# Kernel tuning notes

Measured on AMD Instinct MI355X. Metric: run time of the kernel, lower is better.

## Reference

```python
import jax, jax.numpy as jnp
import numpy as np

N = 100000   # nodes
E = 800000   # edges
D = 64       # feature dim (input=hidden=output)
EPS = 1e-5   # BatchNorm eps


def setup_inputs() -> dict:
    key = jax.random.key(0)
    ks = jax.random.split(key, 24)
    s = 1.0 / np.sqrt(D)
    inp = {
        "x": jax.random.normal(ks[0], (N, D), jnp.float32),
        "edge_index": jax.random.randint(ks[1], (2, E), 0, N, jnp.int64),
        # GCNConv weights (x @ W + b after normalized aggregation)
        "W1": jax.random.normal(ks[2], (D, D), jnp.float32) * s,
        "b1": jax.random.normal(ks[3], (D,), jnp.float32) * 0.01,
        "W2": jax.random.normal(ks[4], (D, D), jnp.float32) * s,
        "b2": jax.random.normal(ks[5], (D,), jnp.float32) * 0.01,
        "W3": jax.random.normal(ks[6], (D, D), jnp.float32) * s,
        "b3": jax.random.normal(ks[7], (D,), jnp.float32) * 0.01,
        # BatchNorm1d (inference: running stats)
        "bn1_g": jax.random.uniform(ks[8], (D,), jnp.float32, 0.5, 1.5),
        "bn1_b": jax.random.normal(ks[9], (D,), jnp.float32) * 0.1,
        "bn1_m": jax.random.normal(ks[10], (D,), jnp.float32) * 0.1,
        "bn1_v": jax.random.uniform(ks[11], (D,), jnp.float32, 0.5, 1.5),
        "bn2_g": jax.random.uniform(ks[12], (D,), jnp.float32, 0.5, 1.5),
        "bn2_b": jax.random.normal(ks[13], (D,), jnp.float32) * 0.1,
        "bn2_m": jax.random.normal(ks[14], (D,), jnp.float32) * 0.1,
        "bn2_v": jax.random.uniform(ks[15], (D,), jnp.float32, 0.5, 1.5),
        # predictor MLP: Linear -> tanh -> (dropout=id) -> Linear
        "pW1": jax.random.normal(ks[16], (D, D), jnp.float32) * s,
        "pb1": jax.random.normal(ks[17], (D,), jnp.float32) * 0.01,
        "pW2": jax.random.normal(ks[18], (D, D), jnp.float32) * s,
        "pb2": jax.random.normal(ks[19], (D,), jnp.float32) * 0.01,
    }
    return inp


def _gcn_norm(edge_index):
    # add self loops, compute sym-normalized edge coefficients (PyG GCNConv)
    loop = jnp.arange(N, dtype=edge_index.dtype)
    src = jnp.concatenate([edge_index[0], loop])
    dst = jnp.concatenate([edge_index[1], loop])
    deg = jax.ops.segment_sum(jnp.ones(src.shape[0], jnp.float32), dst, num_segments=N)
    dis = jax.lax.rsqrt(deg)  # deg >= 1 due to self loops
    norm = dis[src] * dis[dst]
    return src, dst, norm


def _gcn_layer(x, src, dst, norm, W, b):
    h = x @ W                              # [N, D] small GEMM
    msg = h[src] * norm[:, None]           # [E+N, D] gather (memory bound)
    return jax.ops.segment_sum(msg, dst, num_segments=N) + b  # scatter-add


def _bn(x, g, b, m, v):
    return (x - m) * (g * jax.lax.rsqrt(v + EPS)) + b


def reference(x, edge_index, W1, b1, W2, b2, W3, b3,
              bn1_g, bn1_b, bn1_m, bn1_v, bn2_g, bn2_b, bn2_m, bn2_v,
              pW1, pb1, pW2, pb2):
    src, dst, norm = _gcn_norm(edge_index)
    h = _gcn_layer(x, src, dst, norm, W1, b1)
    h = jax.nn.relu(_bn(h, bn1_g, bn1_b, bn1_m, bn1_v))   # dropout = id (eval)
    h = _gcn_layer(h, src, dst, norm, W2, b2)
    h = jax.nn.relu(_bn(h, bn2_g, bn2_b, bn2_m, bn2_v))
    h = _gcn_layer(h, src, dst, norm, W3, b3)
    out = jnp.tanh(h @ pW1 + pb1) @ pW2 + pb2              # predictor MLP
    return out
```

## Files before the change

kernel.cpp:

```cpp
#include <hip/hip_runtime.h>
#include <hip/hip_fp16.h>

#define N_NODES 100000
#define N_EDGES 800000
#define DIM 64
#define BN_EPS 1e-5f
#define LDX 68
#define EDGE_CAP 1600000

__global__ __launch_bounds__(256) void k_cvt_count(const float* __restrict__ x,
                                                   __half* __restrict__ xh,
                                                   const int* __restrict__ dst,
                                                   int* __restrict__ deg,
                                                   int* __restrict__ rank) {
    int idx = blockIdx.x * blockDim.x + threadIdx.x;
    if (idx < 1600000) {
        float4 v = ((const float4*)x)[idx];
        unsigned int u0 = __half_as_ushort(__float2half(v.x));
        unsigned int u1 = __half_as_ushort(__float2half(v.y));
        unsigned int u2 = __half_as_ushort(__float2half(v.z));
        unsigned int u3 = __half_as_ushort(__float2half(v.w));
        ((uint2*)xh)[idx] = make_uint2(u0 | (u1 << 16), u2 | (u3 << 16));
    }
    if (idx < N_EDGES) rank[idx] = atomicAdd(&deg[dst[idx]], 1);
}

__global__ __launch_bounds__(256) void k_scan_fuse(const int* __restrict__ deg,
                                                   int* __restrict__ row_off,
                                                   float* __restrict__ dinv,
                                                   int* __restrict__ gcount,
                                                   const float* __restrict__ W3,
                                                   const float* __restrict__ b3,
                                                   const float* __restrict__ pW1,
                                                   const float* __restrict__ pb1,
                                                   float* __restrict__ W3p,
                                                   float* __restrict__ b3p) {
    int tid = threadIdx.x;
    if (blockIdx.x == 98) {
        int c = tid & 63;
        int kbase = (tid >> 6) * 16;
        for (int k = kbase; k < kbase + 16; ++k) {
            float acc = 0.f;
#pragma unroll 8
            for (int j = 0; j < 64; ++j)
                acc = fmaf(W3[k * 64 + j], pW1[j * 64 + c], acc);
            W3p[k * 64 + c] = acc;
        }
        if (tid < 64) {
            float acc = pb1[c];
#pragma unroll 8
            for (int j = 0; j < 64; ++j)
                acc = fmaf(b3[j], pW1[j * 64 + c], acc);
            b3p[c] = acc;
        }
        return;
    }
    __shared__ int sdata[256];
    __shared__ int sbase;
    int base = blockIdx.x * 1024 + tid * 4;
    int4 d = make_int4(0, 0, 0, 0);
    int4 v = make_int4(0, 0, 0, 0);
    if (base < N_NODES) {
        d = *(const int4*)(deg + base);
        v.x = (d.x + 7) & ~7;
        v.y = (d.y + 7) & ~7;
        v.z = (d.z + 7) & ~7;
        v.w = (d.w + 7) & ~7;
    }
    int tsum = v.x + v.y + v.z + v.w;
    sdata[tid] = tsum;
    __syncthreads();
    for (int off = 1; off < 256; off <<= 1) {
        int t = (tid >= off) ? sdata[tid - off] : 0;
        __syncthreads();
        sdata[tid] += t;
        __syncthreads();
    }
    if (tid == 255) sbase = atomicAdd(gcount, sdata[255]);
    __syncthreads();
    if (base >= N_NODES) return;
    int excl = sdata[tid] - tsum + sbase;
    int4 o;
    o.x = excl;
    o.y = o.x + v.x;
    o.z = o.y + v.y;
    o.w = o.z + v.z;
    *(int4*)(row_off + base) = o;
    float4 di;
    di.x = rsqrtf((float)(d.x + 1));
    di.y = rsqrtf((float)(d.y + 1));
    di.z = rsqrtf((float)(d.z + 1));
    di.w = rsqrtf((float)(d.w + 1));
    *(float4*)(dinv + base) = di;
}

__global__ __launch_bounds__(256) void k_build(const int* __restrict__ ei,
                                               const int* __restrict__ rank,
                                               const int* __restrict__ row_off,
                                               const float* __restrict__ dinv,
                                               int2* __restrict__ edges) {
    int idx = blockIdx.x * 256 + threadIdx.x;
    if (idx >= 200000) return;
    int4 s4 = ((const int4*)ei)[idx];
    int4 d4 = ((const int4*)(ei + N_EDGES))[idx];
    int4 r4 = ((const int4*)rank)[idx];
    edges[row_off[d4.x] + r4.x] = make_int2(s4.x, __float_as_int(dinv[s4.x] * dinv[d4.x]));
    edges[row_off[d4.y] + r4.y] = make_int2(s4.y, __float_as_int(dinv[s4.y] * dinv[d4.y]));
    edges[row_off[d4.z] + r4.z] = make_int2(s4.z, __float_as_int(dinv[s4.z] * dinv[d4.z]));
    edges[row_off[d4.w] + r4.w] = make_int2(s4.w, __float_as_int(dinv[s4.w] * dinv[d4.w]));
}

__global__ __launch_bounds__(256) void k_aggregate(const __half* __restrict__ xin,
                                                   const int* __restrict__ row_off,
                                                   const int* __restrict__ deg,
                                                   const int2* __restrict__ edges,
                                                   const float* __restrict__ dinv,
                                                   __half* __restrict__ out) {
    int lane16 = threadIdx.x & 15;
    int node = blockIdx.x * 16 + (threadIdx.x >> 4);
    float di = dinv[node];
    int beg = row_off[node];
    int len = deg[node];

    uint2 us = ((const uint2*)(xin + (size_t)node * DIM))[lane16];
    float w0 = di * di;
    float4 acc;
    acc.x = __half2float(__ushort_as_half((unsigned short)(us.x & 0xffff))) * w0;
    acc.y = __half2float(__ushort_as_half((unsigned short)(us.x >> 16))) * w0;
    acc.z = __half2float(__ushort_as_half((unsigned short)(us.y & 0xffff))) * w0;
    acc.w = __half2float(__ushort_as_half((unsigned short)(us.y >> 16))) * w0;

    int lenmax = len;
    lenmax = max(lenmax, __shfl_xor(lenmax, 16, 64));
    lenmax = max(lenmax, __shfl_xor(lenmax, 32, 64));

    int lclamp = (len > 0) ? (len - 1) : 0;
    for (int i = 0; i < lenmax; i += 8) {
#pragma unroll
        for (int u = 0; u < 8; ++u) {
            int j = i + u;
            int jc = j < lclamp ? j : lclamp;
            int2 e = edges[beg + jc];
            int s = ((unsigned)e.x < N_NODES) ? e.x : 0;
            float w = (j < len) ? __int_as_float(e.y) : 0.f;
            uint2 u2 = ((const uint2*)(xin + (size_t)s * DIM))[lane16];
            acc.x = fmaf(w, __half2float(__ushort_as_half((unsigned short)(u2.x & 0xffff))), acc.x);
            acc.y = fmaf(w, __half2float(__ushort_as_half((unsigned short)(u2.x >> 16))), acc.y);
            acc.z = fmaf(w, __half2float(__ushort_as_half((unsigned short)(u2.y & 0xffff))), acc.z);
            acc.w = fmaf(w, __half2float(__ushort_as_half((unsigned short)(u2.y >> 16))), acc.w);
        }
    }

    unsigned int p0 = __half_as_ushort(__float2half(acc.x)) |
                      (__half_as_ushort(__float2half(acc.y)) << 16);
    unsigned int p1 = __half_as_ushort(__float2half(acc.z)) |
                      (__half_as_ushort(__float2half(acc.w)) << 16);
    ((uint2*)(out + (size_t)node * DIM))[lane16] = make_uint2(p0, p1);
}

#define GEMM_STEP(SX, SW)                                                      \
    {                                                                          \
        float4 a0 = *(const float4*)&SX[(r0 + 0) * LDX + k4 * 4];              \
        float4 a1 = *(const float4*)&SX[(r0 + 1) * LDX + k4 * 4];              \
        float4 a2 = *(const float4*)&SX[(r0 + 2) * LDX + k4 * 4];              \
        float4 a3 = *(const float4*)&SX[(r0 + 3) * LDX + k4 * 4];              \
        float4 b0 = *(const float4*)&SW[(k4 * 4 + 0) * 64 + c0];               \
        float4 b1 = *(const float4*)&SW[(k4 * 4 + 1) * 64 + c0];               \
        float4 b2 = *(const float4*)&SW[(k4 * 4 + 2) * 64 + c0];               \
        float4 b3 = *(const float4*)&SW[(k4 * 4 + 3) * 64 + c0];               \
        const float* ap[4] = {&a0.x, &a1.x, &a2.x, &a3.x};                     \
        _Pragma("unroll") for (int i = 0; i < 4; ++i) {                        \
            float x0 = ap[i][0], x1 = ap[i][1], x2 = ap[i][2], x3 = ap[i][3];  \
            acc[i][0] = fmaf(x0, b0.x, acc[i][0]);                             \
            acc[i][1] = fmaf(x0, b0.y, acc[i][1]);                             \
            acc[i][2] = fmaf(x0, b0.z, acc[i][2]);                             \
            acc[i][3] = fmaf(x0, b0.w, acc[i][3]);                             \
            acc[i][0] = fmaf(x1, b1.x, acc[i][0]);                             \
            acc[i][1] = fmaf(x1, b1.y, acc[i][1]);                             \
            acc[i][2] = fmaf(x1, b1.z, acc[i][2]);                             \
            acc[i][3] = fmaf(x1, b1.w, acc[i][3]);                             \
            acc[i][0] = fmaf(x2, b2.x, acc[i][0]);                             \
            acc[i][1] = fmaf(x2, b2.y, acc[i][1]);                             \
            acc[i][2] = fmaf(x2, b2.z, acc[i][2]);                             \
            acc[i][3] = fmaf(x2, b2.w, acc[i][3]);                             \
            acc[i][0] = fmaf(x3, b3.x, acc[i][0]);                             \
            acc[i][1] = fmaf(x3, b3.y, acc[i][1]);                             \
            acc[i][2] = fmaf(x3, b3.z, acc[i][2]);                             \
            acc[i][3] = fmaf(x3, b3.w, acc[i][3]);                             \
        }                                                                      \
    }

#define STAGE_H2F(SRCPTR, SXPTR)                                               \
    {                                                                          \
        int r = tid >> 2;                                                      \
        int q = tid & 3;                                                       \
        int row = row0 + r;                                                    \
        float4* dst = (float4*)(SXPTR + r * LDX);                              \
        if (row < N_NODES) {                                                   \
            const uint2* src = (const uint2*)(SRCPTR + (size_t)row * DIM);     \
            _Pragma("unroll") for (int m = 0; m < 4; ++m) {                    \
                uint2 u = src[q + m * 4];                                      \
                float4 f;                                                      \
                f.x = __half2float(__ushort_as_half((unsigned short)(u.x & 0xffff)));       \
                f.y = __half2float(__ushort_as_half((unsigned short)(u.x >> 16)));          \
                f.z = __half2float(__ushort_as_half((unsigned short)(u.y & 0xffff)));       \
                f.w = __half2float(__ushort_as_half((unsigned short)(u.y >> 16)));          \
                dst[q + m * 4] = f;                                            \
            }                                                                  \
        } else {                                                               \
            float4 z = make_float4(0.f, 0.f, 0.f, 0.f);                        \
            _Pragma("unroll") for (int m = 0; m < 4; ++m) dst[q + m * 4] = z;  \
        }                                                                      \
    }

__global__ __launch_bounds__(256) void k_gemm_bn_h(const __half* __restrict__ xin,
                                                   const float* __restrict__ W,
                                                   const float* __restrict__ bias,
                                                   const float* __restrict__ bng,
                                                   const float* __restrict__ bnb,
                                                   const float* __restrict__ bnm,
                                                   const float* __restrict__ bnv,
                                                   __half* __restrict__ out) {
    __shared__ float sW[4096];
    __shared__ float sX[64 * LDX];
    int tid = threadIdx.x;
    int row0 = blockIdx.x * 64;

    for (int i = tid; i < 1024; i += 256)
        ((float4*)sW)[i] = ((const float4*)W)[i];
    STAGE_H2F(xin, sX)
    __syncthreads();

    int cq = tid & 15, rq = tid >> 4;
    int c0 = cq * 4, r0 = rq * 4;
    float acc[4][4];
#pragma unroll
    for (int i = 0; i < 4; ++i)
#pragma unroll
        for (int j = 0; j < 4; ++j) acc[i][j] = 0.f;

#pragma unroll 4
    for (int k4 = 0; k4 < 16; ++k4) GEMM_STEP(sX, sW)

    float4 bv = *(const float4*)&bias[c0];
    float4 g = *(const float4*)&bng[c0];
    float4 bb = *(const float4*)&bnb[c0];
    float4 m = *(const float4*)&bnm[c0];
    float4 vv = *(const float4*)&bnv[c0];
    float A0 = g.x * rsqrtf(vv.x + BN_EPS);
    float A1 = g.y * rsqrtf(vv.y + BN_EPS);
    float A2 = g.z * rsqrtf(vv.z + BN_EPS);
    float A3 = g.w * rsqrtf(vv.w + BN_EPS);
    float B0 = (bv.x - m.x) * A0 + bb.x;
    float B1 = (bv.y - m.y) * A1 + bb.y;
    float B2 = (bv.z - m.z) * A2 + bb.z;
    float B3 = (bv.w - m.w) * A3 + bb.w;
#pragma unroll
    for (int i = 0; i < 4; ++i) {
        int row = row0 + r0 + i;
        if (row >= N_NODES) break;
        unsigned int u0 = __half_as_ushort(__float2half(fmaxf(0.f, fmaf(acc[i][0], A0, B0))));
        unsigned int u1 = __half_as_ushort(__float2half(fmaxf(0.f, fmaf(acc[i][1], A1, B1))));
        unsigned int u2 = __half_as_ushort(__float2half(fmaxf(0.f, fmaf(acc[i][2], A2, B2))));
        unsigned int u3 = __half_as_ushort(__float2half(fmaxf(0.f, fmaf(acc[i][3], A3, B3))));
        *(uint2*)(out + (size_t)row * DIM + c0) = make_uint2(u0 | (u1 << 16), u2 | (u3 << 16));
    }
}

__global__ __launch_bounds__(256) void k_tail(const __half* __restrict__ xin,
                                              const float* __restrict__ W3p,
                                              const float* __restrict__ b3p,
                                              const float* __restrict__ pW2,
                                              const float* __restrict__ pb2,
                                              float* __restrict__ out) {
    __shared__ float sW1[4096];
    __shared__ float sW2[4096];
    __shared__ float sX[64 * LDX];
    int tid = threadIdx.x;
    int row0 = blockIdx.x * 64;

    for (int i = tid; i < 1024; i += 256) {
        ((float4*)sW1)[i] = ((const float4*)W3p)[i];
        ((float4*)sW2)[i] = ((const float4*)pW2)[i];
    }
    STAGE_H2F(xin, sX)
    __syncthreads();

    int cq = tid & 15, rq = tid >> 4;
    int c0 = cq * 4, r0 = rq * 4;
    float acc[4][4];

#pragma unroll
    for (int i = 0; i < 4; ++i)
#pragma unroll
        for (int j = 0; j < 4; ++j) acc[i][j] = 0.f;
#pragma unroll 4
    for (int k4 = 0; k4 < 16; ++k4) GEMM_STEP(sX, sW1)
    __syncthreads();

    {
        float4 bv = *(const float4*)&b3p[c0];
#pragma unroll
        for (int i = 0; i < 4; ++i) {
            float4 h;
            h.x = tanhf(acc[i][0] + bv.x);
            h.y = tanhf(acc[i][1] + bv.y);
            h.z = tanhf(acc[i][2] + bv.z);
            h.w = tanhf(acc[i][3] + bv.w);
            *(float4*)&sX[(r0 + i) * LDX + c0] = h;
        }
    }
    __syncthreads();

#pragma unroll
    for (int i = 0; i < 4; ++i)
#pragma unroll
        for (int j = 0; j < 4; ++j) acc[i][j] = 0.f;
#pragma unroll 4
    for (int k4 = 0; k4 < 16; ++k4) GEMM_STEP(sX, sW2)

    float4 bv = *(const float4*)&pb2[c0];
#pragma unroll
    for (int i = 0; i < 4; ++i) {
        int row = row0 + r0 + i;
        if (row >= N_NODES) break;
        float4 o;
        o.x = acc[i][0] + bv.x;
        o.y = acc[i][1] + bv.y;
        o.z = acc[i][2] + bv.z;
        o.w = acc[i][3] + bv.w;
        *(float4*)(out + (size_t)row * DIM + c0) = o;
    }
}

extern "C" void kernel_launch(void* const* d_in, const int* in_sizes, int n_in,
                              void* d_out, int out_size, void* d_ws, size_t ws_size,
                              hipStream_t stream) {
    const float* x     = (const float*)d_in[0];
    const int*   ei    = (const int*)d_in[1];
    const float* W1    = (const float*)d_in[2];
    const float* b1    = (const float*)d_in[3];
    const float* W2    = (const float*)d_in[4];
    const float* b2    = (const float*)d_in[5];
    const float* W3    = (const float*)d_in[6];
    const float* b3    = (const float*)d_in[7];
    const float* bn1_g = (const float*)d_in[8];
    const float* bn1_b = (const float*)d_in[9];
    const float* bn1_m = (const float*)d_in[10];
    const float* bn1_v = (const float*)d_in[11];
    const float* bn2_g = (const float*)d_in[12];
    const float* bn2_b = (const float*)d_in[13];
    const float* bn2_m = (const float*)d_in[14];
    const float* bn2_v = (const float*)d_in[15];
    const float* pW1   = (const float*)d_in[16];
    const float* pb1   = (const float*)d_in[17];
    const float* pW2   = (const float*)d_in[18];
    const float* pb2   = (const float*)d_in[19];
    float* out = (float*)d_out;

    char* ws = (char*)d_ws;
    int*    deg     = (int*)ws;                      ws += 100352 * 4;
    int*    gcount  = (int*)ws;                      ws += 4 * 4;
    int*    row_off = (int*)ws;                      ws += 100352 * 4;
    int*    rank    = (int*)ws;                      ws += (size_t)N_EDGES * 4;
    int2*   edges   = (int2*)ws;                     ws += (size_t)EDGE_CAP * 8;
    float*  dinv    = (float*)ws;                    ws += 100352 * 4;
    float*  W3p     = (float*)ws;                    ws += 4096 * 4;
    float*  b3p     = (float*)ws;                    ws += 64 * 4;
    __half* xh      = (__half*)ws;                   ws += (size_t)N_NODES * DIM * 2;
    __half* hbuf    = (__half*)ws;                   ws += (size_t)N_NODES * DIM * 2;
    __half* abuf    = (__half*)ws;                   ws += (size_t)N_NODES * DIM * 2;

    const int blk = 256;
    int gCvt   = 6250;
    int gBuild = 782;
    int gAgg   = N_NODES / 16;
    int gTile  = (N_NODES + 63) / 64;

    hipMemsetAsync(deg, 0, (size_t)(100352 + 4) * 4, stream);
    k_cvt_count<<<gCvt, blk, 0, stream>>>(x, xh, ei + N_EDGES, deg, rank);
    k_scan_fuse<<<99, blk, 0, stream>>>(deg, row_off, dinv, gcount,
                                        W3, b3, pW1, pb1, W3p, b3p);
    k_build<<<gBuild, blk, 0, stream>>>(ei, rank, row_off, dinv, edges);

    k_aggregate<<<gAgg, blk, 0, stream>>>(xh, row_off, deg, edges, dinv, abuf);
    k_gemm_bn_h<<<gTile, blk, 0, stream>>>(abuf, W1, b1, bn1_g, bn1_b, bn1_m, bn1_v, hbuf);

    k_aggregate<<<gAgg, blk, 0, stream>>>(hbuf, row_off, deg, edges, dinv, abuf);
    k_gemm_bn_h<<<gTile, blk, 0, stream>>>(abuf, W2, b2, bn2_g, bn2_b, bn2_m, bn2_v, hbuf);

    k_aggregate<<<gAgg, blk, 0, stream>>>(hbuf, row_off, deg, edges, dinv, abuf);
    k_tail<<<gTile, blk, 0, stream>>>(abuf, W3p, b3p, pW2, pb2, out);
}
```

Before: 369.2 us.

## Use 8 lanes per node with 16-byte gathers and prefetch next edge batch

The aggregation kernel now gives each node 8 lanes instead of 16, so each lane loads a uint4 (8 halves) per neighbor row and 32 nodes are handled per block. The edge records for the next batch of 8 are software-prefetched into registers while the current batch's feature gathers are issued. The aim is fewer, wider memory transactions and hidden edge-list latency in this memory-bound scatter/gather. In exchange, registers per thread go up and there are fewer lanes per node, which could lower occupancy or leave lanes idle when degrees within a wavefront differ.

```diff
diff --git a/kernel.cpp b/kernel.cpp
--- a/kernel.cpp
+++ b/kernel.cpp
@@ -7,6 +7,9 @@
 #define BN_EPS 1e-5f
 #define LDX 68
 #define EDGE_CAP 1600000
+
+#define H2F_LO(u) __half2float(__ushort_as_half((unsigned short)((u) & 0xffff)))
+#define H2F_HI(u) __half2float(__ushort_as_half((unsigned short)((u) >> 16)))
 
 __global__ __launch_bounds__(256) void k_cvt_count(const float* __restrict__ x,
                                                    __half* __restrict__ xh,
@@ -116,46 +119,77 @@
                                                    const int2* __restrict__ edges,
                                                    const float* __restrict__ dinv,
                                                    __half* __restrict__ out) {
-    int lane16 = threadIdx.x & 15;
-    int node = blockIdx.x * 16 + (threadIdx.x >> 4);
+    int lane8 = threadIdx.x & 7;
+    int node = blockIdx.x * 32 + (threadIdx.x >> 3);
     float di = dinv[node];
     int beg = row_off[node];
     int len = deg[node];
 
-    uint2 us = ((const uint2*)(xin + (size_t)node * DIM))[lane16];
+    uint4 us = ((const uint4*)(xin + (size_t)node * DIM))[lane8];
     float w0 = di * di;
-    float4 acc;
-    acc.x = __half2float(__ushort_as_half((unsigned short)(us.x & 0xffff))) * w0;
-    acc.y = __half2float(__ushort_as_half((unsigned short)(us.x >> 16))) * w0;
-    acc.z = __half2float(__ushort_as_half((unsigned short)(us.y & 0xffff))) * w0;
-    acc.w = __half2float(__ushort_as_half((unsigned short)(us.y >> 16))) * w0;
+    float acc[8];
+    acc[0] = H2F_LO(us.x) * w0;
+    acc[1] = H2F_HI(us.x) * w0;
+    acc[2] = H2F_LO(us.y) * w0;
+    acc[3] = H2F_HI(us.y) * w0;
+    acc[4] = H2F_LO(us.z) * w0;
+    acc[5] = H2F_HI(us.z) * w0;
+    acc[6] = H2F_LO(us.w) * w0;
+    acc[7] = H2F_HI(us.w) * w0;
 
     int lenmax = len;
+    lenmax = max(lenmax, __shfl_xor(lenmax, 8, 64));
     lenmax = max(lenmax, __shfl_xor(lenmax, 16, 64));
     lenmax = max(lenmax, __shfl_xor(lenmax, 32, 64));
 
     int lclamp = (len > 0) ? (len - 1) : 0;
-    for (int i = 0; i < lenmax; i += 8) {
+    if (lenmax > 0) {
+        int2 e[8];
 #pragma unroll
         for (int u = 0; u < 8; ++u) {
-            int j = i + u;
-            int jc = j < lclamp ? j : lclamp;
-            int2 e = edges[beg + jc];
-            int s = ((unsigned)e.x < N_NODES) ? e.x : 0;
-            float w = (j < len) ? __int_as_float(e.y) : 0.f;
-            uint2 u2 = ((const uint2*)(xin + (size_t)s * DIM))[lane16];
-            acc.x = fmaf(w, __half2float(__ushort_as_half((unsigned short)(u2.x & 0xffff))), acc.x);
-            acc.y = fmaf(w, __half2float(__ushort_as_half((unsigned short)(u2.x >> 16))), acc.y);
-            acc.z = fmaf(w, __half2float(__ushort_as_half((unsigned short)(u2.y & 0xffff))), acc.z);
-            acc.w = fmaf(w, __half2float(__ushort_as_half((unsigned short)(u2.y >> 16))), acc.w);
+            int jc = (u < lclamp) ? u : lclamp;
+            e[u] = edges[beg + jc];
         }
-    }
-
-    unsigned int p0 = __half_as_ushort(__float2half(acc.x)) |
-                      (__half_as_ushort(__float2half(acc.y)) << 16);
-    unsigned int p1 = __half_as_ushort(__float2half(acc.z)) |
-                      (__half_as_ushort(__float2half(acc.w)) << 16);
-    ((uint2*)(out + (size_t)node * DIM))[lane16] = make_uint2(p0, p1);
+        for (int i = 0; i < lenmax; i += 8) {
+            int2 en[8];
+            int inext = i + 8;
+            if (inext < lenmax) {
+#pragma unroll
+                for (int u = 0; u < 8; ++u) {
+                    int j = inext + u;
+                    int jc = (j < lclamp) ? j : lclamp;
+                    en[u] = edges[beg + jc];
+                }
+            } else {
+#pragma unroll
+                for (int u = 0; u < 8; ++u) en[u] = e[u];
+            }
+#pragma unroll
+            for (int u = 0; u < 8; ++u) {
+                int j = i + u;
+                int s = ((unsigned)e[u].x < N_NODES) ? e[u].x : 0;
+                float w = (j < len) ? __int_as_float(e[u].y) : 0.f;
+                uint4 g = ((const uint4*)(xin + (size_t)s * DIM))[lane8];
+                acc[0] = fmaf(w, H2F_LO(g.x), acc[0]);
+                acc[1] = fmaf(w, H2F_HI(g.x), acc[1]);
+                acc[2] = fmaf(w, H2F_LO(g.y), acc[2]);
+                acc[3] = fmaf(w, H2F_HI(g.y), acc[3]);
+                acc[4] = fmaf(w, H2F_LO(g.z), acc[4]);
+                acc[5] = fmaf(w, H2F_HI(g.z), acc[5]);
+                acc[6] = fmaf(w, H2F_LO(g.w), acc[6]);
+                acc[7] = fmaf(w, H2F_HI(g.w), acc[7]);
+            }
+#pragma unroll
+            for (int u = 0; u < 8; ++u) e[u] = en[u];
+        }
+    }
+
+    uint4 p;
+    p.x = __half_as_ushort(__float2half(acc[0])) | (__half_as_ushort(__float2half(acc[1])) << 16);
+    p.y = __half_as_ushort(__float2half(acc[2])) | (__half_as_ushort(__float2half(acc[3])) << 16);
+    p.z = __half_as_ushort(__float2half(acc[4])) | (__half_as_ushort(__float2half(acc[5])) << 16);
+    p.w = __half_as_ushort(__float2half(acc[6])) | (__half_as_ushort(__float2half(acc[7])) << 16);
+    ((uint4*)(out + (size_t)node * DIM))[lane8] = p;
 }
 
 #define GEMM_STEP(SX, SW)                                                      \
@@ -201,10 +235,10 @@
             _Pragma("unroll") for (int m = 0; m < 4; ++m) {                    \
                 uint2 u = src[q + m * 4];                                      \
                 float4 f;                                                      \
-                f.x = __half2float(__ushort_as_half((unsigned short)(u.x & 0xffff)));       \
-                f.y = __half2float(__ushort_as_half((unsigned short)(u.x >> 16)));          \
-                f.z = __half2float(__ushort_as_half((unsigned short)(u.y & 0xffff)));       \
-                f.w = __half2float(__ushort_as_half((unsigned short)(u.y >> 16)));          \
+                f.x = H2F_LO(u.x);                                             \
+                f.y = H2F_HI(u.x);                                             \
+                f.z = H2F_LO(u.y);                                             \
+                f.w = H2F_HI(u.y);                                             \
                 dst[q + m * 4] = f;                                            \
             }                                                                  \
         } else {                                                               \
@@ -374,7 +408,7 @@
     const int blk = 256;
     int gCvt   = 6250;
     int gBuild = 782;
-    int gAgg   = N_NODES / 16;
+    int gAgg   = N_NODES / 32;
     int gTile  = (N_NODES + 63) / 64;
 
     hipMemsetAsync(deg, 0, (size_t)(100352 + 4) * 4, stream);
```

New measurement: 339.7 us (median of 3 runs). 8.0% less time.
